# Performance work log

Measured on AMD Instinct MI355X. Metric: run time of the kernel, lower is better.

The kernel has to match this reference:

```python
import jax, jax.numpy as jnp
import numpy as np

DIM = 128
EDGE_FEAT_DIM = 2
N_NODES = 50000
N_EDGES = 600000
EPS = 1e-5


def setup_inputs() -> dict:
    key = jax.random.key(0)
    ks = jax.random.split(key, 16)
    d = DIM
    inp = {}
    inp["x"] = jax.random.normal(ks[0], (N_NODES, d), dtype=jnp.float32)
    inp["edge_index"] = jax.random.randint(ks[1], (2, N_EDGES), 0, N_NODES, dtype=jnp.int32)
    inp["edge_weight_norm"] = jax.random.uniform(ks[2], (N_EDGES,), dtype=jnp.float32)
    inp["edge_feat"] = jax.random.normal(ks[3], (N_EDGES, EDGE_FEAT_DIM), dtype=jnp.float32)
    inp["batch"] = jnp.zeros((N_NODES,), dtype=jnp.int32)
    # phi: Linear(dim, dim)
    inp["W_phi"] = jax.random.normal(ks[4], (d, d), dtype=jnp.float32) * (1.0 / np.sqrt(d))
    inp["b_phi"] = jnp.zeros((d,), dtype=jnp.float32)
    # edge_gate: Linear(2d+2, d) -> BN(d) -> GELU -> Linear(d, 1)
    din = 2 * d + EDGE_FEAT_DIM
    inp["W_g1"] = jax.random.normal(ks[5], (din, d), dtype=jnp.float32) * (1.0 / np.sqrt(din))
    inp["b_g1"] = jnp.zeros((d,), dtype=jnp.float32)
    inp["bn_gamma"] = jnp.ones((d,), dtype=jnp.float32)
    inp["bn_beta"] = jnp.zeros((d,), dtype=jnp.float32)
    inp["bn_mean"] = jnp.zeros((d,), dtype=jnp.float32)
    inp["bn_var"] = jnp.ones((d,), dtype=jnp.float32)
    inp["W_g2"] = jax.random.normal(ks[6], (d, 1), dtype=jnp.float32) * (1.0 / np.sqrt(d))
    inp["b_g2"] = jnp.zeros((1,), dtype=jnp.float32)
    # upd: Linear(2d, d)
    inp["W_u"] = jax.random.normal(ks[7], (2 * d, d), dtype=jnp.float32) * (1.0 / np.sqrt(2 * d))
    inp["b_u"] = jnp.zeros((d,), dtype=jnp.float32)
    # LayerNorm(dim)
    inp["ln_gamma"] = jnp.ones((d,), dtype=jnp.float32)
    inp["ln_beta"] = jnp.zeros((d,), dtype=jnp.float32)
    return inp


def reference(x, edge_index, edge_weight_norm, edge_feat, batch,
              W_phi, b_phi, W_g1, b_g1, bn_gamma, bn_beta, bn_mean, bn_var,
              W_g2, b_g2, W_u, b_u, ln_gamma, ln_beta):
    src, dst = edge_index[0], edge_index[1]
    # phi(x): [N, d]
    xj = x @ W_phi + b_phi
    # edge gate MLP on [x_dst, x_src, e]: [E, 2d+2]
    g_in = jnp.concatenate([x[dst], x[src], edge_feat], axis=-1)
    h1 = g_in @ W_g1 + b_g1
    h1 = (h1 - bn_mean) * jax.lax.rsqrt(bn_var + EPS) * bn_gamma + bn_beta  # BN eval mode
    h1 = jax.nn.gelu(h1, approximate=False)
    gate = jax.nn.sigmoid(h1 @ W_g2 + b_g2)[:, 0]  # [E]
    # messages and scatter-add aggregation
    msg = xj[src] * (edge_weight_norm * gate)[:, None]  # [E, d]
    agg = jax.ops.segment_sum(msg, dst, num_segments=x.shape[0])  # [N, d]
    # update MLP + GELU + residual + LayerNorm
    h = jnp.concatenate([x, agg], axis=-1) @ W_u + b_u
    h = jax.nn.gelu(h, approximate=False)
    y = x + h
    mu = jnp.mean(y, axis=-1, keepdims=True)
    var = jnp.var(y, axis=-1, keepdims=True)
    return (y - mu) * jax.lax.rsqrt(var + EPS) * ln_gamma + ln_beta
```

## Files before the change

kernel.cpp:

```cpp
#include <hip/hip_runtime.h>
#include <hip/hip_fp16.h>
#include <math.h>

#define DIM 128
#define NN 50000
#define NE 600000
#define EPS 1e-5f
#define CAP 64

struct H8 { __half2 h[4]; };
struct F8 { float4 a, b; };

typedef _Float16 f16x8 __attribute__((ext_vector_type(8)));
typedef float    f32x4 __attribute__((ext_vector_type(4)));

__device__ __forceinline__ float gelu_fast(float x) {
    const float c1 = 2.3022085f;
    const float c2 = 0.1029437f;
    const float x2 = x * x;
    const float z  = x * __builtin_fmaf(c2, x2, c1);
    const float u  = __builtin_amdgcn_exp2f(z);
    const float r  = __builtin_amdgcn_rcpf(1.f + u);
    return __builtin_fmaf(-x, r, x);
}

__device__ __forceinline__ float sigmoid_fast(float y) {
    const float u = __builtin_amdgcn_exp2f(-1.4426950409f * y);
    return __builtin_amdgcn_rcpf(1.f + u);
}

__global__ __launch_bounds__(256) void k_prep_scale(
    const float* __restrict__ Wg1, const float* __restrict__ bg1,
    const float* __restrict__ bng, const float* __restrict__ bnb,
    const float* __restrict__ bnm, const float* __restrict__ bnv,
    __half* __restrict__ WABth, float* __restrict__ bA,
    float* __restrict__ w0p, float* __restrict__ w1p)
{
    const int k = blockIdx.x;
    const int t = threadIdx.x;
    const int c = t & 127;
    const float s = bng[c] * rsqrtf(bnv[c] + EPS);
    const float w = (t < 128) ? Wg1[k * DIM + c] : Wg1[(DIM + k) * DIM + c];
    WABth[t * DIM + k] = __float2half(w * s);
    if (k == 0 && t < 128) {
        const float tt = bnb[c] - bnm[c] * s;
        bA[c]  = bg1[c] * s + tt;
        w0p[c] = Wg1[256 * DIM + c] * s;
        w1p[c] = Wg1[257 * DIM + c] * s;
    }
}

__global__ __launch_bounds__(128) void k_prep_wpu(
    const float* __restrict__ Wphi, const float* __restrict__ bphi,
    const float* __restrict__ Wu,
    __half* __restrict__ Wct, float* __restrict__ bpu)
{
    const int a = blockIdx.x;
    const int j = threadIdx.x;
    float acc = 0.f;
    #pragma unroll 8
    for (int k = 0; k < DIM; ++k)
        acc += Wphi[a * DIM + k] * Wu[(DIM + k) * DIM + j];
    Wct[j * 256 + a]       = __float2half(Wu[a * DIM + j]);
    Wct[j * 256 + 128 + a] = __float2half(acc);
    if (a == 0) {
        float b = 0.f;
        #pragma unroll 8
        for (int k = 0; k < DIM; ++k)
            b += bphi[k] * Wu[(DIM + k) * DIM + j];
        bpu[j] = b;
    }
}

__global__ __launch_bounds__(256) void k_node_mfma(
    const float* __restrict__ x, const __half* __restrict__ WABth,
    const float* __restrict__ bA,
    __half* __restrict__ A, __half* __restrict__ Bv, __half* __restrict__ xh)
{
    __shared__ __half tile[64][264];
    const int t    = threadIdx.x;
    const int wv   = t >> 6;
    const int lane = t & 63;
    const int n16  = lane & 15;
    const int quad = lane >> 4;
    const int m0   = blockIdx.x * 64;

    f32x4 acc[4][4];
    #pragma unroll
    for (int mt = 0; mt < 4; ++mt)
        #pragma unroll
        for (int nt = 0; nt < 4; ++nt)
            acc[mt][nt] = (f32x4){0.f, 0.f, 0.f, 0.f};

    int rowm[4];
    #pragma unroll
    for (int mt = 0; mt < 4; ++mt)
        rowm[mt] = min(m0 + mt * 16 + n16, NN - 1);

    #pragma unroll
    for (int ks = 0; ks < 4; ++ks) {
        const int ko = ks * 32 + quad * 8;
        f16x8 bf[4];
        #pragma unroll
        for (int nt = 0; nt < 4; ++nt) {
            const int c = wv * 64 + nt * 16 + n16;
            bf[nt] = *(const f16x8*)(WABth + c * DIM + ko);
        }
        #pragma unroll
        for (int mt = 0; mt < 4; ++mt) {
            const float4 xa = *(const float4*)(x + (size_t)rowm[mt] * DIM + ko);
            const float4 xb = *(const float4*)(x + (size_t)rowm[mt] * DIM + ko + 4);
            f16x8 af;
            af[0] = (_Float16)xa.x; af[1] = (_Float16)xa.y;
            af[2] = (_Float16)xa.z; af[3] = (_Float16)xa.w;
            af[4] = (_Float16)xb.x; af[5] = (_Float16)xb.y;
            af[6] = (_Float16)xb.z; af[7] = (_Float16)xb.w;
            if (wv == 0)
                *(f16x8*)(xh + (size_t)rowm[mt] * DIM + ko) = af;
            #pragma unroll
            for (int nt = 0; nt < 4; ++nt)
                acc[mt][nt] = __builtin_amdgcn_mfma_f32_16x16x32_f16(
                    af, bf[nt], acc[mt][nt], 0, 0, 0);
        }
    }

    #pragma unroll
    for (int nt = 0; nt < 4; ++nt) {
        const int c = wv * 64 + nt * 16 + n16;
        const float bias = (c < 128) ? bA[c] : 0.f;
        #pragma unroll
        for (int mt = 0; mt < 4; ++mt)
            #pragma unroll
            for (int reg = 0; reg < 4; ++reg)
                tile[mt * 16 + quad * 4 + reg][c] =
                    __float2half(acc[mt][nt][reg] + bias);
    }
    __syncthreads();

    #pragma unroll
    for (int i = 0; i < 8; ++i) {
        const int chunk = t + i * 256;
        const int row = chunk >> 5;
        const int o   = (chunk & 31) * 8;
        if (m0 + row < NN) {
            const uint4 v = *(const uint4*)&tile[row][o];
            if (o < 128) *(uint4*)(A  + (size_t)(m0 + row) * DIM + o)       = v;
            else         *(uint4*)(Bv + (size_t)(m0 + row) * DIM + o - 128) = v;
        }
    }
}

__global__ __launch_bounds__(256) void k_gate(
    const int*   __restrict__ ei,  const float* __restrict__ ew,
    const float* __restrict__ ef,
    const __half* __restrict__ A,  const __half* __restrict__ Bv,
    const float* __restrict__ w0p, const float* __restrict__ w1p,
    const float* __restrict__ Wg2, const float* __restrict__ bg2,
    int* __restrict__ deg, int2* __restrict__ pairs)
{
    const int t    = threadIdx.x;
    const int lane = t & 63;
    const int sub  = lane >> 4;
    const int sl   = lane & 15;
    const int c8   = sl * 8;
    const int e0   = (blockIdx.x * 4 + (t >> 6)) * 8 + sub * 2;

    const F8 WG = *(const F8*)(Wg2 + c8);
    const F8 W0 = *(const F8*)(w0p + c8);
    const F8 W1 = *(const F8*)(w1p + c8);
    const float bg2v = bg2[0];
    const float* w0 = (const float*)&W0;
    const float* w1 = (const float*)&W1;
    const float* wg = (const float*)&WG;

    const int2   srcs = *(const int2*)(ei + e0);
    const int2   dsts = *(const int2*)(ei + NE + e0);
    const float4 efv  = *(const float4*)(ef + 2 * e0);
    const float2 ewv  = *(const float2*)(ew + e0);

    const H8 a0 = *(const H8*)(A  + (size_t)dsts.x * DIM + c8);
    const H8 b0 = *(const H8*)(Bv + (size_t)srcs.x * DIM + c8);
    const H8 a1 = *(const H8*)(A  + (size_t)dsts.y * DIM + c8);
    const H8 b1 = *(const H8*)(Bv + (size_t)srcs.y * DIM + c8);

    float p0 = 0.f, p1 = 0.f;
    #pragma unroll
    for (int i = 0; i < 4; ++i) {
        const float2 s0 = __half22float2(__hadd2(a0.h[i], b0.h[i]));
        const float2 s1 = __half22float2(__hadd2(a1.h[i], b1.h[i]));
        const int c0 = 2 * i, c1 = 2 * i + 1;
        float h;
        h = s0.x + efv.x * w0[c0] + efv.y * w1[c0];
        p0 = __builtin_fmaf(gelu_fast(h), wg[c0], p0);
        h = s0.y + efv.x * w0[c1] + efv.y * w1[c1];
        p0 = __builtin_fmaf(gelu_fast(h), wg[c1], p0);
        h = s1.x + efv.z * w0[c0] + efv.w * w1[c0];
        p1 = __builtin_fmaf(gelu_fast(h), wg[c0], p1);
        h = s1.y + efv.z * w0[c1] + efv.w * w1[c1];
        p1 = __builtin_fmaf(gelu_fast(h), wg[c1], p1);
    }
    #pragma unroll
    for (int off = 1; off < 16; off <<= 1) {
        p0 += __shfl_xor(p0, off, 64);
        p1 += __shfl_xor(p1, off, 64);
    }

    if (sl == 0) {
        const float coef0 = ewv.x * sigmoid_fast(p0 + bg2v);
        const float coef1 = ewv.y * sigmoid_fast(p1 + bg2v);
        const int pos0 = atomicAdd(&deg[dsts.x], 1);
        if (pos0 < CAP)
            pairs[(size_t)dsts.x * CAP + pos0] = make_int2(srcs.x, __float_as_int(coef0));
        const int pos1 = atomicAdd(&deg[dsts.y], 1);
        if (pos1 < CAP)
            pairs[(size_t)dsts.y * CAP + pos1] = make_int2(srcs.y, __float_as_int(coef1));
    }
}

__global__ __launch_bounds__(256) void k_agg_update(
    const int* __restrict__ deg, const int2* __restrict__ pairs,
    const __half* __restrict__ xh, const __half* __restrict__ Wct,
    const float* __restrict__ bu, const float* __restrict__ bpu,
    const float* __restrict__ lng, const float* __restrict__ lnb,
    float* __restrict__ out)
{
    __shared__ __half xt[64][136];
    __shared__ __half at[64][136];
    __shared__ float sct[64];

    const int t    = threadIdx.x;
    const int wv   = t >> 6;
    const int lane = t & 63;
    const int n16  = lane & 15;
    const int quad = lane >> 4;
    const int m0   = blockIdx.x * 64;

    const int slot = t >> 4;
    const int sl   = t & 15;
    const int c8   = sl * 8;

    int    dd[4];
    size_t bb[4];
    #pragma unroll
    for (int r = 0; r < 4; ++r) {
        const int lr = r * 16 + slot;
        const int nc = min(m0 + lr, NN - 1);
        dd[r] = min(deg[nc], CAP);
        bb[r] = (size_t)nc * CAP;
    }

    #pragma unroll
    for (int i = 0; i < 4; ++i) {
        const int idx = i * 256 + t;
        const int row = idx >> 4;
        const int col = (idx & 15) * 8;
        const int grow = min(m0 + row, NN - 1);
        *(f16x8*)&xt[row][col] = *(const f16x8*)(xh + (size_t)grow * DIM + col);
    }

    float acc[4][8];
    float scn[4] = {0.f, 0.f, 0.f, 0.f};
    #pragma unroll
    for (int r = 0; r < 4; ++r)
        #pragma unroll
        for (int i = 0; i < 8; ++i) acc[r][i] = 0.f;

    const int dmax = max(max(dd[0], dd[1]), max(dd[2], dd[3]));

    for (int j = 0; j < dmax; j += 2) {
        int4 pq[4];
        #pragma unroll
        for (int r = 0; r < 4; ++r)
            pq[r] = *(const int4*)(&pairs[bb[r] + j]);

        int   ix[8];
        float cf[8];
        #pragma unroll
        for (int r = 0; r < 4; ++r) {
            const bool v0 = (j     < dd[r]);
            const bool v1 = (j + 1 < dd[r]);
            ix[2 * r]     = v0 ? pq[r].x : 0;
            cf[2 * r]     = v0 ? __int_as_float(pq[r].y) : 0.f;
            ix[2 * r + 1] = v1 ? pq[r].z : 0;
            cf[2 * r + 1] = v1 ? __int_as_float(pq[r].w) : 0.f;
        }

        H8 xv[8];
        #pragma unroll
        for (int q = 0; q < 8; ++q)
            xv[q] = *(const H8*)(xh + (size_t)ix[q] * DIM + c8);

        #pragma unroll
        for (int r = 0; r < 4; ++r) {
            #pragma unroll
            for (int k = 0; k < 2; ++k) {
                const int   q  = 2 * r + k;
                const float c  = cf[q];
                #pragma unroll
                for (int i = 0; i < 4; ++i) {
                    const float2 f = __half22float2(xv[q].h[i]);
                    acc[r][2 * i]     = __builtin_fmaf(c, f.x, acc[r][2 * i]);
                    acc[r][2 * i + 1] = __builtin_fmaf(c, f.y, acc[r][2 * i + 1]);
                }
                scn[r] += c;
            }
        }
    }

    #pragma unroll
    for (int r = 0; r < 4; ++r) {
        const int lr = r * 16 + slot;
        f16x8 hv;
        #pragma unroll
        for (int i = 0; i < 8; ++i) hv[i] = (_Float16)acc[r][i];
        *(f16x8*)&at[lr][c8] = hv;
        if (sl == 0) sct[lr] = scn[r];
    }
    __syncthreads();

    f32x4 acc2[8];
    #pragma unroll
    for (int nt = 0; nt < 8; ++nt) acc2[nt] = (f32x4){0.f, 0.f, 0.f, 0.f};

    const int rloc = wv * 16 + n16;
    #pragma unroll
    for (int ks = 0; ks < 4; ++ks) {
        const int ko = ks * 32 + quad * 8;
        const f16x8 af = *(const f16x8*)&xt[rloc][ko];
        #pragma unroll
        for (int nt = 0; nt < 8; ++nt) {
            const f16x8 bf = *(const f16x8*)(Wct + (nt * 16 + n16) * 256 + ko);
            acc2[nt] = __builtin_amdgcn_mfma_f32_16x16x32_f16(af, bf, acc2[nt], 0, 0, 0);
        }
    }
    #pragma unroll
    for (int ks = 0; ks < 4; ++ks) {
        const int ko = ks * 32 + quad * 8;
        const f16x8 af = *(const f16x8*)&at[rloc][ko];
        #pragma unroll
        for (int nt = 0; nt < 8; ++nt) {
            const f16x8 bf = *(const f16x8*)(Wct + (nt * 16 + n16) * 256 + 128 + ko);
            acc2[nt] = __builtin_amdgcn_mfma_f32_16x16x32_f16(af, bf, acc2[nt], 0, 0, 0);
        }
    }

    int   rl[4];
    float scv[4];
    #pragma unroll
    for (int reg = 0; reg < 4; ++reg) {
        rl[reg]  = wv * 16 + quad * 4 + reg;
        scv[reg] = sct[rl[reg]];
    }

    float yv[8][4];
    float s[4]  = {0.f, 0.f, 0.f, 0.f};
    float ss[4] = {0.f, 0.f, 0.f, 0.f};

    #pragma unroll
    for (int nt = 0; nt < 8; ++nt) {
        const int c = nt * 16 + n16;
        const float buv = bu[c], bpv = bpu[c];
        #pragma unroll
        for (int reg = 0; reg < 4; ++reg) {
            float h = acc2[nt][reg] + buv + scv[reg] * bpv;
            h = gelu_fast(h);
            const float xv = __half2float(xt[rl[reg]][c]);
            const float y = xv + h;
            yv[nt][reg] = y;
            s[reg]  += y;
            ss[reg] += y * y;
        }
    }

    #pragma unroll
    for (int reg = 0; reg < 4; ++reg) {
        #pragma unroll
        for (int off = 1; off < 16; off <<= 1) {
            s[reg]  += __shfl_xor(s[reg],  off, 64);
            ss[reg] += __shfl_xor(ss[reg], off, 64);
        }
    }

    float mu[4], rs[4];
    #pragma unroll
    for (int reg = 0; reg < 4; ++reg) {
        mu[reg] = s[reg] * (1.f / DIM);
        const float var = ss[reg] * (1.f / DIM) - mu[reg] * mu[reg];
        rs[reg] = rsqrtf(var + EPS);
    }

    #pragma unroll
    for (int nt = 0; nt < 8; ++nt) {
        const int c = nt * 16 + n16;
        const float gg = lng[c], bb2 = lnb[c];
        #pragma unroll
        for (int reg = 0; reg < 4; ++reg) {
            const int grow = m0 + rl[reg];
            if (grow < NN)
                __builtin_nontemporal_store(
                    (yv[nt][reg] - mu[reg]) * rs[reg] * gg + bb2,
                    &out[(size_t)grow * DIM + c]);
        }
    }
}

extern "C" void kernel_launch(void* const* d_in, const int* in_sizes, int n_in,
                              void* d_out, int out_size, void* d_ws, size_t ws_size,
                              hipStream_t stream)
{
    const float* x    = (const float*)d_in[0];
    const int*   ei   = (const int*)  d_in[1];
    const float* ew   = (const float*)d_in[2];
    const float* ef   = (const float*)d_in[3];
    const float* Wphi = (const float*)d_in[5];
    const float* bphi = (const float*)d_in[6];
    const float* Wg1  = (const float*)d_in[7];
    const float* bg1  = (const float*)d_in[8];
    const float* bng  = (const float*)d_in[9];
    const float* bnb  = (const float*)d_in[10];
    const float* bnm  = (const float*)d_in[11];
    const float* bnv  = (const float*)d_in[12];
    const float* Wg2  = (const float*)d_in[13];
    const float* bg2  = (const float*)d_in[14];
    const float* Wu   = (const float*)d_in[15];
    const float* bu   = (const float*)d_in[16];
    const float* lng  = (const float*)d_in[17];
    const float* lnb  = (const float*)d_in[18];

    float* out = (float*)d_out;

    char* wsb = (char*)d_ws;
    size_t off = 0;
    auto carve = [&](size_t bytes) -> void* {
        void* p = wsb + off;
        off += (bytes + 255) & ~(size_t)255;
        return p;
    };
    __half* xh    = (__half*)carve((size_t)NN * DIM * 2);
    __half* A     = (__half*)carve((size_t)NN * DIM * 2);
    __half* Bv    = (__half*)carve((size_t)NN * DIM * 2);
    __half* WABth = (__half*)carve(256 * DIM * 2);
    __half* Wct   = (__half*)carve(DIM * 256 * 2);
    float*  bA    = (float*) carve(DIM * 4);
    float*  w0p   = (float*) carve(DIM * 4);
    float*  w1p   = (float*) carve(DIM * 4);
    float*  bpu   = (float*) carve(DIM * 4);
    int*    deg   = (int*)   carve((size_t)NN * 4);
    int2*   pairs = (int2*)  carve((size_t)NN * CAP * 8);

    hipMemsetAsync(deg, 0, (size_t)NN * 4, stream);

    k_prep_scale<<<128, 256, 0, stream>>>(Wg1, bg1, bng, bnb, bnm, bnv,
                                          WABth, bA, w0p, w1p);
    k_prep_wpu<<<128, 128, 0, stream>>>(Wphi, bphi, Wu, Wct, bpu);
    k_node_mfma<<<(NN + 63) / 64, 256, 0, stream>>>(x, WABth, bA, A, Bv, xh);
    k_gate<<<NE / 32, 256, 0, stream>>>(ei, ew, ef, A, Bv, w0p, w1p, Wg2, bg2,
                                        deg, pairs);
    k_agg_update<<<(NN + 63) / 64, 256, 0, stream>>>(deg, pairs, xh, Wct,
                                                     bu, bpu, lng, lnb, out);
}
```

Baseline: 276.6 us.

## Shrink aggregate-update blocks to one wave and gather four neighbours per step

Measured after the change: 263.6 us. 4.7% less time.

```diff
diff --git a/kernel.cpp b/kernel.cpp
--- a/kernel.cpp
+++ b/kernel.cpp
@@ -217,23 +217,21 @@
     }
 }
 
-__global__ __launch_bounds__(256) void k_agg_update(
+__global__ __launch_bounds__(64, 3) void k_agg_update(
     const int* __restrict__ deg, const int2* __restrict__ pairs,
     const __half* __restrict__ xh, const __half* __restrict__ Wct,
     const float* __restrict__ bu, const float* __restrict__ bpu,
     const float* __restrict__ lng, const float* __restrict__ lnb,
     float* __restrict__ out)
 {
-    __shared__ __half xt[64][136];
-    __shared__ __half at[64][136];
-    __shared__ float sct[64];
+    __shared__ __half xt[16][136];
+    __shared__ __half at[16][136];
+    __shared__ float sct[16];
 
     const int t    = threadIdx.x;
-    const int wv   = t >> 6;
-    const int lane = t & 63;
-    const int n16  = lane & 15;
-    const int quad = lane >> 4;
-    const int m0   = blockIdx.x * 64;
+    const int n16  = t & 15;
+    const int quad = t >> 4;
+    const int m0   = blockIdx.x * 16;
 
     const int slot = t >> 4;
     const int sl   = t & 15;
@@ -243,7 +241,7 @@
     size_t bb[4];
     #pragma unroll
     for (int r = 0; r < 4; ++r) {
-        const int lr = r * 16 + slot;
+        const int lr = r * 4 + slot;
         const int nc = min(m0 + lr, NN - 1);
         dd[r] = min(deg[nc], CAP);
         bb[r] = (size_t)nc * CAP;
@@ -251,7 +249,7 @@
 
     #pragma unroll
     for (int i = 0; i < 4; ++i) {
-        const int idx = i * 256 + t;
+        const int idx = i * 64 + t;
         const int row = idx >> 4;
         const int col = (idx & 15) * 8;
         const int grow = min(m0 + row, NN - 1);
@@ -267,35 +265,44 @@
 
     const int dmax = max(max(dd[0], dd[1]), max(dd[2], dd[3]));
 
-    for (int j = 0; j < dmax; j += 2) {
-        int4 pq[4];
-        #pragma unroll
-        for (int r = 0; r < 4; ++r)
-            pq[r] = *(const int4*)(&pairs[bb[r] + j]);
-
-        int   ix[8];
-        float cf[8];
+    for (int j = 0; j < dmax; j += 4) {
+        int4 pq0[4], pq1[4];
         #pragma unroll
         for (int r = 0; r < 4; ++r) {
+            pq0[r] = *(const int4*)(&pairs[bb[r] + j]);
+            pq1[r] = *(const int4*)(&pairs[bb[r] + j + 2]);
+        }
+
+        int   ix[16];
+        float cf[16];
+        #pragma unroll
+        for (int r = 0; r < 4; ++r) {
+            const int q = 4 * r;
             const bool v0 = (j     < dd[r]);
             const bool v1 = (j + 1 < dd[r]);
-            ix[2 * r]     = v0 ? pq[r].x : 0;
-            cf[2 * r]     = v0 ? __int_as_float(pq[r].y) : 0.f;
-            ix[2 * r + 1] = v1 ? pq[r].z : 0;
-            cf[2 * r + 1] = v1 ? __int_as_float(pq[r].w) : 0.f;
-        }
-
-        H8 xv[8];
-        #pragma unroll
-        for (int q = 0; q < 8; ++q)
+            const bool v2 = (j + 2 < dd[r]);
+            const bool v3 = (j + 3 < dd[r]);
+            ix[q]     = v0 ? pq0[r].x : 0;
+            cf[q]     = v0 ? __int_as_float(pq0[r].y) : 0.f;
+            ix[q + 1] = v1 ? pq0[r].z : 0;
+            cf[q + 1] = v1 ? __int_as_float(pq0[r].w) : 0.f;
+            ix[q + 2] = v2 ? pq1[r].x : 0;
+            cf[q + 2] = v2 ? __int_as_float(pq1[r].y) : 0.f;
+            ix[q + 3] = v3 ? pq1[r].z : 0;
+            cf[q + 3] = v3 ? __int_as_float(pq1[r].w) : 0.f;
+        }
+
+        H8 xv[16];
+        #pragma unroll
+        for (int q = 0; q < 16; ++q)
             xv[q] = *(const H8*)(xh + (size_t)ix[q] * DIM + c8);
 
         #pragma unroll
         for (int r = 0; r < 4; ++r) {
             #pragma unroll
-            for (int k = 0; k < 2; ++k) {
-                const int   q  = 2 * r + k;
-                const float c  = cf[q];
+            for (int k = 0; k < 4; ++k) {
+                const int   q = 4 * r + k;
+                const float c = cf[q];
                 #pragma unroll
                 for (int i = 0; i < 4; ++i) {
                     const float2 f = __half22float2(xv[q].h[i]);
@@ -309,7 +316,7 @@
 
     #pragma unroll
     for (int r = 0; r < 4; ++r) {
-        const int lr = r * 16 + slot;
+        const int lr = r * 4 + slot;
         f16x8 hv;
         #pragma unroll
         for (int i = 0; i < 8; ++i) hv[i] = (_Float16)acc[r][i];
@@ -322,7 +329,7 @@
     #pragma unroll
     for (int nt = 0; nt < 8; ++nt) acc2[nt] = (f32x4){0.f, 0.f, 0.f, 0.f};
 
-    const int rloc = wv * 16 + n16;
+    const int rloc = n16;
     #pragma unroll
     for (int ks = 0; ks < 4; ++ks) {
         const int ko = ks * 32 + quad * 8;
@@ -348,7 +355,7 @@
     float scv[4];
     #pragma unroll
     for (int reg = 0; reg < 4; ++reg) {
-        rl[reg]  = wv * 16 + quad * 4 + reg;
+        rl[reg]  = quad * 4 + reg;
         scv[reg] = sct[rl[reg]];
     }
 
@@ -446,7 +453,7 @@
     float*  w1p   = (float*) carve(DIM * 4);
     float*  bpu   = (float*) carve(DIM * 4);
     int*    deg   = (int*)   carve((size_t)NN * 4);
-    int2*   pairs = (int2*)  carve((size_t)NN * CAP * 8);
+    int2*   pairs = (int2*)  carve((size_t)NN * CAP * 8 + 256);
 
     hipMemsetAsync(deg, 0, (size_t)NN * 4, stream);
 
@@ -456,6 +463,6 @@
     k_node_mfma<<<(NN + 63) / 64, 256, 0, stream>>>(x, WABth, bA, A, Bv, xh);
     k_gate<<<NE / 32, 256, 0, stream>>>(ei, ew, ef, A, Bv, w0p, w1p, Wg2, bg2,
                                         deg, pairs);
-    k_agg_update<<<(NN + 63) / 64, 256, 0, stream>>>(deg, pairs, xh, Wct,
-                                                     bu, bpu, lng, lnb, out);
-}
+    k_agg_update<<<(NN + 15) / 16, 64, 0, stream>>>(deg, pairs, xh, Wct,
+                                                    bu, bpu, lng, lnb, out);
+}
```
